# Performance work log

Measured on AMD Instinct MI355X. Metric: run time of the kernel, lower is better.

## Reference

```python
import jax, jax.numpy as jnp
import numpy as np

N_NODES = 50000   # nodes per channel
N_EDGES = 800000  # intra edges per channel (avg degree ~16)
N_GRAPHS = 64     # graphs in the batch (global_add_pool segments)
D = 128           # node_features_len == out_channels
L = 3             # n_layers
BN_EPS = 1e-5
NEG_SLOPE = 0.01  # F.leaky_relu default


def setup_inputs() -> dict:
    key = jax.random.key(0)
    ks = jax.random.split(key, 24)
    s = 0.05
    inp = {
        "x1": jax.random.normal(ks[0], (N_NODES, D), jnp.float32),
        "x2": jax.random.normal(ks[1], (N_NODES, D), jnp.float32),
        # GIN MLP channel 1: Linear-BN-ReLU-Linear-ReLU, stacked over layers
        "W1_ch1": jax.random.normal(ks[2], (L, D, D), jnp.float32) * s,
        "b1_ch1": jax.random.normal(ks[3], (L, D), jnp.float32) * s,
        "bn_g": 1.0 + jax.random.normal(ks[4], (L, D), jnp.float32) * s,
        "bn_b": jax.random.normal(ks[5], (L, D), jnp.float32) * s,
        "bn_m": jax.random.normal(ks[6], (L, D), jnp.float32) * s,
        "bn_v": 0.5 + jax.random.uniform(ks[7], (L, D), jnp.float32),
        "W2_ch1": jax.random.normal(ks[8], (L, D, D), jnp.float32) * s,
        "b2_ch1": jax.random.normal(ks[9], (L, D), jnp.float32) * s,
        # GIN MLP channel 2: Linear-ReLU-Linear
        "W1_ch2": jax.random.normal(ks[10], (L, D, D), jnp.float32) * s,
        "b1_ch2": jax.random.normal(ks[11], (L, D), jnp.float32) * s,
        "W2_ch2": jax.random.normal(ks[12], (L, D, D), jnp.float32) * s,
        "b2_ch2": jax.random.normal(ks[13], (L, D), jnp.float32) * s,
        # head: Linear(2*D*L -> D) - ReLU - Dropout - Linear(D -> 1)
        "Wf1": jax.random.normal(ks[14], (2 * D * L, D), jnp.float32) * s,
        "bf1": jax.random.normal(ks[15], (D,), jnp.float32) * s,
        "Wf2": jax.random.normal(ks[16], (D, 1), jnp.float32) * s,
        "bf2": jax.random.normal(ks[17], (1,), jnp.float32) * s,
        "edge1": jax.random.randint(ks[18], (2, N_EDGES), 0, N_NODES, dtype=jnp.int32),
        "edge2": jax.random.randint(ks[19], (2, N_EDGES), 0, N_NODES, dtype=jnp.int32),
        "batch1": jnp.sort(jax.random.randint(ks[20], (N_NODES,), 0, N_GRAPHS, dtype=jnp.int32)),
        "batch2": jnp.sort(jax.random.randint(ks[21], (N_NODES,), 0, N_GRAPHS, dtype=jnp.int32)),
    }
    return inp


def _aggregate(x, edge):
    # GINConv sum aggregation: message x[src] scattered to dst; eps=0 default
    return jax.ops.segment_sum(x[edge[0]], edge[1], num_segments=N_NODES)


def _channel1(x, edge, batch, W1, b1, g, b, m, v, W2, b2):
    pooled = []
    for i in range(L):
        h = (x + _aggregate(x, edge)) @ W1[i] + b1[i]
        h = (h - m[i]) * (g[i] / jnp.sqrt(v[i] + BN_EPS)) + b[i]  # eval-mode BN
        h = jax.nn.relu(h)
        h = jax.nn.relu(h @ W2[i] + b2[i])
        x = jax.nn.leaky_relu(h, NEG_SLOPE)
        pooled.append(jax.ops.segment_sum(x, batch, num_segments=N_GRAPHS))
    return jnp.concatenate(pooled, axis=-1)  # [G, D*L]


def _channel2(x, edge, batch, W1, b1, W2, b2):
    pooled = []
    for i in range(L):
        h = jax.nn.relu((x + _aggregate(x, edge)) @ W1[i] + b1[i])
        h = h @ W2[i] + b2[i]
        x = jax.nn.leaky_relu(h, NEG_SLOPE)
        pooled.append(jax.ops.segment_sum(x, batch, num_segments=N_GRAPHS))
    return jnp.concatenate(pooled, axis=-1)  # [G, D*L]


def reference(x1, x2, W1_ch1, b1_ch1, bn_g, bn_b, bn_m, bn_v, W2_ch1, b2_ch1,
              W1_ch2, b1_ch2, W2_ch2, b2_ch2, Wf1, bf1, Wf2, bf2,
              edge1, edge2, batch1, batch2):
    p1 = _channel1(x1, edge1, batch1, W1_ch1, b1_ch1, bn_g, bn_b, bn_m, bn_v, W2_ch1, b2_ch1)
    p2 = _channel2(x2, edge2, batch2, W1_ch2, b1_ch2, W2_ch2, b2_ch2)
    z = jnp.concatenate([p1, p2], axis=-1)  # [G, 2*D*L]
    h = jax.nn.relu(z @ Wf1 + bf1)          # dropout is identity in eval mode
    return h @ Wf2 + bf2                    # [G, 1]
```

## Files before the change

kernel.cpp:

```cpp
#include <hip/hip_runtime.h>

#define NN 50000
#define NE 800000
#define NG 64
#define DD 128
#define NL 3
#define ZW (2 * DD * NL)
#define NB2 128
#define NPB 391
#define CAP2 8192
#define CHUNK 4096
#define P1B 196

typedef __attribute__((ext_vector_type(8))) short short8;
typedef __attribute__((ext_vector_type(4))) float f32x4;

__device__ inline unsigned short f2bf(float f) {
  unsigned int u = __float_as_uint(f);
  unsigned int r = (u + 0x7fffu + ((u >> 16) & 1u)) >> 16;
  return (unsigned short)r;
}

__global__ __launch_bounds__(256) void cvt_bf16_kernel(const float* __restrict__ in,
                                                       unsigned short* __restrict__ out, int n8) {
  int i = blockIdx.x * 256 + threadIdx.x;
  if (i >= n8) return;
  const float4* in4 = reinterpret_cast<const float4*>(in);
  float4 a = in4[2 * i], b = in4[2 * i + 1];
  uint4 o;
  o.x = (unsigned int)f2bf(a.x) | ((unsigned int)f2bf(a.y) << 16);
  o.y = (unsigned int)f2bf(a.z) | ((unsigned int)f2bf(a.w) << 16);
  o.z = (unsigned int)f2bf(b.x) | ((unsigned int)f2bf(b.y) << 16);
  o.w = (unsigned int)f2bf(b.z) | ((unsigned int)f2bf(b.w) << 16);
  reinterpret_cast<uint4*>(out)[i] = o;
}

__global__ __launch_bounds__(256) void cvt_wt_kernel(const float* __restrict__ in,
                                                     unsigned short* __restrict__ out) {
  __shared__ float tile[32][33];
  int mat = blockIdx.z;
  int k0 = blockIdx.x * 32, c0 = blockIdx.y * 32;
  int tx = threadIdx.x & 31, ty = threadIdx.x >> 5;
  const float* ip = in + mat * 16384;
  unsigned short* op = out + mat * 16384;
#pragma unroll
  for (int rr = 0; rr < 32; rr += 8)
    tile[ty + rr][tx] = ip[(k0 + ty + rr) * 128 + (c0 + tx)];
  __syncthreads();
#pragma unroll
  for (int rr = 0; rr < 32; rr += 8)
    op[(c0 + ty + rr) * 128 + (k0 + tx)] = f2bf(tile[tx][ty + rr]);
}

__global__ __launch_bounds__(256) void bucket_kernel(const int* __restrict__ e1,
                                                     const int* __restrict__ e2,
                                                     int* __restrict__ bcur,
                                                     uint2* __restrict__ pairs) {
  int ch = blockIdx.x >= P1B;
  int blk = blockIdx.x - ch * P1B;
  const int* E = ch ? e2 : e1;
  int base = blk * CHUNK;
  __shared__ int lcnt[NB2], gbase[NB2];
  for (int i = threadIdx.x; i < NB2; i += 256) lcnt[i] = 0;
  __syncthreads();
  int srcv[16], dstv[16], lrank[16];
#pragma unroll
  for (int k = 0; k < 16; k++) {
    int e = base + k * 256 + threadIdx.x;
    if (e < NE) {
      srcv[k] = E[e];
      dstv[k] = E[NE + e];
      lrank[k] = atomicAdd(&lcnt[dstv[k] / NPB], 1);
    } else dstv[k] = -1;
  }
  __syncthreads();
  for (int i = threadIdx.x; i < NB2; i += 256)
    gbase[i] = atomicAdd(&bcur[ch * NB2 + i], lcnt[i]);
  __syncthreads();
#pragma unroll
  for (int k = 0; k < 16; k++)
    if (dstv[k] >= 0) {
      int g = dstv[k] / NPB;
      pairs[(size_t)(ch * NB2 + g) * CAP2 + gbase[g] + lrank[k]] =
          make_uint2((unsigned)srcv[k], (unsigned)dstv[k]);
    }
}

__global__ __launch_bounds__(256) void scan_bcur_kernel(const int* __restrict__ bcur,
                                                        int* __restrict__ colbase) {
  __shared__ int s[256];
  int tid = threadIdx.x;
  int v = bcur[tid];
  s[tid] = v;
  __syncthreads();
  int segstart = tid & ~127;
  for (int o = 1; o < 128; o <<= 1) {
    int t = (tid - o >= segstart) ? s[tid - o] : 0;
    __syncthreads();
    s[tid] += t;
    __syncthreads();
  }
  colbase[tid] = s[tid] - v;
}

__global__ __launch_bounds__(256) void csr_build_kernel(const uint2* __restrict__ pairs,
                                                        const int* __restrict__ bcur,
                                                        const int* __restrict__ colbase,
                                                        int* __restrict__ rowptr,
                                                        int* __restrict__ col) {
  int g = blockIdx.x;
  int ch = g >> 7, b = g & 127;
  int node0 = b * NPB;
  int nloc = min(NPB, NN - node0);
  int count = bcur[g];
  int base = colbase[g];
  const uint2* p = pairs + (size_t)g * CAP2;
  __shared__ int hist[512], pref[512], cur[512], stmp[256];
  for (int i = threadIdx.x; i < 512; i += 256) hist[i] = 0;
  __syncthreads();
  for (int e = threadIdx.x; e < count; e += 256)
    atomicAdd(&hist[(int)p[e].y - node0], 1);
  __syncthreads();
  int t = threadIdx.x;
  int a0 = hist[2 * t], a1 = hist[2 * t + 1];
  int sum = a0 + a1;
  stmp[t] = sum;
  __syncthreads();
  for (int o = 1; o < 256; o <<= 1) {
    int tv = (t >= o) ? stmp[t - o] : 0;
    __syncthreads();
    stmp[t] += tv;
    __syncthreads();
  }
  int ex = stmp[t] - sum;
  pref[2 * t] = ex;       pref[2 * t + 1] = ex + a0;
  cur[2 * t] = ex;        cur[2 * t + 1] = ex + a0;
  __syncthreads();
  for (int i = threadIdx.x; i < nloc; i += 256)
    rowptr[ch * (NN + 1) + node0 + i] = base + pref[i];
  if (threadIdx.x == 0 && b == NB2 - 1) rowptr[ch * (NN + 1) + NN] = base + count;
  for (int e = threadIdx.x; e < count; e += 256) {
    uint2 pr = p[e];
    int pos = atomicAdd(&cur[(int)pr.y - node0], 1);
    col[ch * NE + base + pos] = (int)pr.x;
  }
}

__global__ __launch_bounds__(256) void agg_kernel(const unsigned short* __restrict__ X,
                                                  const int* __restrict__ rowptr,
                                                  const int* __restrict__ col,
                                                  unsigned short* __restrict__ Y) {
  int node = blockIdx.x * 16 + (threadIdx.x >> 4);
  int lane = threadIdx.x & 15;
  int ch = node >= NN;
  int nl = node - ch * NN;
  const int* rp = rowptr + ch * (NN + 1);
  const int* cl = col + ch * NE;
  const uint4* X4 = reinterpret_cast<const uint4*>(X);
  size_t chbase = (size_t)ch * NN * 16;
  float acc[8];
  {
    uint4 sv = X4[(size_t)node * 16 + lane];
    unsigned int w[4] = {sv.x, sv.y, sv.z, sv.w};
#pragma unroll
    for (int q = 0; q < 4; q++) {
      acc[2 * q]     = __uint_as_float(w[q] << 16);
      acc[2 * q + 1] = __uint_as_float(w[q] & 0xffff0000u);
    }
  }
  int s = rp[nl], e = rp[nl + 1];
  int j = s;
  for (; j + 8 <= e; j += 8) {
    uint4 v[8];
#pragma unroll
    for (int q = 0; q < 8; q++)
      v[q] = X4[chbase + (size_t)cl[j + q] * 16 + lane];
#pragma unroll
    for (int q = 0; q < 8; q++) {
      unsigned int w[4] = {v[q].x, v[q].y, v[q].z, v[q].w};
#pragma unroll
      for (int t = 0; t < 4; t++) {
        acc[2 * t]     += __uint_as_float(w[t] << 16);
        acc[2 * t + 1] += __uint_as_float(w[t] & 0xffff0000u);
      }
    }
  }
  for (; j < e; ++j) {
    uint4 v = X4[chbase + (size_t)cl[j] * 16 + lane];
    unsigned int w[4] = {v.x, v.y, v.z, v.w};
#pragma unroll
    for (int t = 0; t < 4; t++) {
      acc[2 * t]     += __uint_as_float(w[t] << 16);
      acc[2 * t + 1] += __uint_as_float(w[t] & 0xffff0000u);
    }
  }
  uint4 o;
  unsigned int* ow = reinterpret_cast<unsigned int*>(&o);
#pragma unroll
  for (int q = 0; q < 4; q++)
    ow[q] = (unsigned int)f2bf(acc[2 * q]) | ((unsigned int)f2bf(acc[2 * q + 1]) << 16);
  reinterpret_cast<uint4*>(Y)[(size_t)node * 16 + lane] = o;
}

__global__ __launch_bounds__(256) void gemm_fused_kernel(
    const unsigned short* __restrict__ Y, unsigned short* __restrict__ X,
    const unsigned short* __restrict__ WT,
    const float* __restrict__ b1c1, const float* __restrict__ b1c2,
    const float* __restrict__ b2c1, const float* __restrict__ b2c2,
    const float* __restrict__ bng, const float* __restrict__ bnb,
    const float* __restrict__ bnm, const float* __restrict__ bnv,
    const int* __restrict__ batch1, const int* __restrict__ batch2,
    float* __restrict__ z, int layer) {
  __shared__ unsigned short hlds[16][136];
  int ch = blockIdx.x >= 1024;
  int lane = threadIdx.x & 63, wv = threadIdx.x >> 6;
  int l15 = lane & 15, lk = lane >> 4;
  int c0 = wv * 32;
  const unsigned short* W1 = WT + (size_t)(ch * 6 + layer) * 16384;
  const unsigned short* W2 = WT + (size_t)(ch * 6 + 3 + layer) * 16384;
  short8 w1f[2][4], w2f[2][4];
#pragma unroll
  for (int ct = 0; ct < 2; ct++)
#pragma unroll
    for (int kk = 0; kk < 4; kk++) {
      size_t boff = (size_t)(c0 + ct * 16 + l15) * 128 + kk * 32 + lk * 8;
      w1f[ct][kk] = *reinterpret_cast<const short8*>(W1 + boff);
      w2f[ct][kk] = *reinterpret_cast<const short8*>(W2 + boff);
    }
  const float* b1 = (ch ? b1c2 : b1c1) + layer * DD;
  const float* b2 = (ch ? b2c2 : b2c1) + layer * DD;
  const int* batch = ch ? batch2 : batch1;
  float sc1[2], sh1[2], sh2[2];
#pragma unroll
  for (int ct = 0; ct < 2; ct++) {
    int colg = c0 + ct * 16 + l15;
    if (!ch) {
      float s = bng[layer * DD + colg] * rsqrtf(bnv[layer * DD + colg] + 1e-5f);
      sc1[ct] = s;
      sh1[ct] = (b1[colg] - bnm[layer * DD + colg]) * s + bnb[layer * DD + colg];
    } else {
      sc1[ct] = 1.f;
      sh1[ct] = b1[colg];
    }
    sh2[ct] = b2[colg];
  }
  for (int t = (ch ? blockIdx.x - 1024 : blockIdx.x); t < 3125; t += 1024) {
    int r0l = t * 16;
    size_t r0g = (size_t)ch * NN + r0l;
    const unsigned short* yp = Y + (r0g + l15) * 128 + lk * 8;
    short8 a0 = *reinterpret_cast<const short8*>(yp);
    short8 a1 = *reinterpret_cast<const short8*>(yp + 32);
    short8 a2 = *reinterpret_cast<const short8*>(yp + 64);
    short8 a3 = *reinterpret_cast<const short8*>(yp + 96);
#pragma unroll
    for (int ct = 0; ct < 2; ct++) {
      f32x4 acc = {0.f, 0.f, 0.f, 0.f};
      acc = __builtin_amdgcn_mfma_f32_16x16x32_bf16(a0, w1f[ct][0], acc, 0, 0, 0);
      acc = __builtin_amdgcn_mfma_f32_16x16x32_bf16(a1, w1f[ct][1], acc, 0, 0, 0);
      acc = __builtin_amdgcn_mfma_f32_16x16x32_bf16(a2, w1f[ct][2], acc, 0, 0, 0);
      acc = __builtin_amdgcn_mfma_f32_16x16x32_bf16(a3, w1f[ct][3], acc, 0, 0, 0);
      int colg = c0 + ct * 16 + l15;
#pragma unroll
      for (int r = 0; r < 4; r++) {
        float tv = fmaxf(acc[r] * sc1[ct] + sh1[ct], 0.f);
        hlds[lk * 4 + r][colg] = f2bf(tv);
      }
    }
    __syncthreads();
    short8 h0 = *reinterpret_cast<const short8*>(&hlds[l15][lk * 8]);
    short8 h1 = *reinterpret_cast<const short8*>(&hlds[l15][32 + lk * 8]);
    short8 h2 = *reinterpret_cast<const short8*>(&hlds[l15][64 + lk * 8]);
    short8 h3 = *reinterpret_cast<const short8*>(&hlds[l15][96 + lk * 8]);
#pragma unroll
    for (int ct = 0; ct < 2; ct++) {
      f32x4 acc = {0.f, 0.f, 0.f, 0.f};
      acc = __builtin_amdgcn_mfma_f32_16x16x32_bf16(h0, w2f[ct][0], acc, 0, 0, 0);
      acc = __builtin_amdgcn_mfma_f32_16x16x32_bf16(h1, w2f[ct][1], acc, 0, 0, 0);
      acc = __builtin_amdgcn_mfma_f32_16x16x32_bf16(h2, w2f[ct][2], acc, 0, 0, 0);
      acc = __builtin_amdgcn_mfma_f32_16x16x32_bf16(h3, w2f[ct][3], acc, 0, 0, 0);
      int colg = c0 + ct * 16 + l15;
      float v[4];
#pragma unroll
      for (int r = 0; r < 4; r++) {
        float tv = acc[r] + sh2[ct];
        if (!ch) tv = fmaxf(tv, 0.f);
        else     tv = tv > 0.f ? tv : 0.01f * tv;
        v[r] = tv;
        X[(r0g + lk * 4 + r) * 128 + colg] = f2bf(tv);
      }
      int zc = ch * (DD * NL) + layer * DD + colg;
      int g0 = batch[r0l], g15 = batch[r0l + 15];
      if (g0 == g15) {
        float s = v[0] + v[1] + v[2] + v[3];
        s += __shfl_xor(s, 16);
        s += __shfl_xor(s, 32);
        if (lk == 0) atomicAdd(&z[(size_t)g0 * ZW + zc], s);
      } else {
#pragma unroll
        for (int r = 0; r < 4; r++)
          atomicAdd(&z[(size_t)batch[r0l + lk * 4 + r] * ZW + zc], v[r]);
      }
    }
    __syncthreads();
  }
}

__global__ __launch_bounds__(128) void head_kernel(const float* __restrict__ z,
                                                   const float* __restrict__ Wf1,
                                                   const float* __restrict__ bf1,
                                                   const float* __restrict__ Wf2,
                                                   const float* __restrict__ bf2,
                                                   float* __restrict__ out) {
  int g = blockIdx.x, t = threadIdx.x;
  const float* zr = z + (size_t)g * ZW;
  float acc = bf1[t];
  for (int j = 0; j < ZW; ++j) acc += zr[j] * Wf1[(size_t)j * DD + t];
  float h = fmaxf(acc, 0.f);
  __shared__ float red[128];
  red[t] = h * Wf2[t];
  __syncthreads();
  for (int s = 64; s > 0; s >>= 1) {
    if (t < s) red[t] += red[t + s];
    __syncthreads();
  }
  if (t == 0) out[g] = red[0] + bf2[0];
}

extern "C" void kernel_launch(void* const* d_in, const int* in_sizes, int n_in,
                              void* d_out, int out_size, void* d_ws, size_t ws_size,
                              hipStream_t stream) {
  const float* x1   = (const float*)d_in[0];
  const float* x2   = (const float*)d_in[1];
  const float* W1c1 = (const float*)d_in[2];
  const float* b1c1 = (const float*)d_in[3];
  const float* bng  = (const float*)d_in[4];
  const float* bnb  = (const float*)d_in[5];
  const float* bnm  = (const float*)d_in[6];
  const float* bnv  = (const float*)d_in[7];
  const float* W2c1 = (const float*)d_in[8];
  const float* b2c1 = (const float*)d_in[9];
  const float* W1c2 = (const float*)d_in[10];
  const float* b1c2 = (const float*)d_in[11];
  const float* W2c2 = (const float*)d_in[12];
  const float* b2c2 = (const float*)d_in[13];
  const float* Wf1  = (const float*)d_in[14];
  const float* bf1  = (const float*)d_in[15];
  const float* Wf2  = (const float*)d_in[16];
  const float* bf2  = (const float*)d_in[17];
  const int* edge1  = (const int*)d_in[18];
  const int* edge2  = (const int*)d_in[19];
  const int* batch1 = (const int*)d_in[20];
  const int* batch2 = (const int*)d_in[21];
  (void)ws_size; (void)n_in; (void)in_sizes; (void)out_size;

  char* ws = (char*)d_ws;
  const size_t NB16 = (size_t)2 * NN * DD * 2;
  unsigned short* bufX = (unsigned short*)(ws);
  unsigned short* bufY = (unsigned short*)(ws + NB16);
  size_t off = 2 * NB16;
  unsigned short* WT = (unsigned short*)(ws + off); off += (size_t)12 * 16384 * 2;
  uint2* pairs = (uint2*)(ws + off); off += (size_t)2 * NB2 * CAP2 * 8;
  int* col     = (int*)(ws + off); off += (size_t)2 * NE * 4;
  int* rowptr  = (int*)(ws + off); off += (((size_t)2 * (NN + 1) * 4) + 255) & ~(size_t)255;
  int* bcur    = (int*)(ws + off); off += 256 * 4;
  int* colbase = (int*)(ws + off); off += 256 * 4;
  float* z     = (float*)(ws + off); off += (size_t)NG * ZW * 4;

  cvt_wt_kernel<<<dim3(4, 4, 3), 256, 0, stream>>>(W1c1, WT + 0 * 16384);
  cvt_wt_kernel<<<dim3(4, 4, 3), 256, 0, stream>>>(W2c1, WT + 3 * 16384);
  cvt_wt_kernel<<<dim3(4, 4, 3), 256, 0, stream>>>(W1c2, WT + 6 * 16384);
  cvt_wt_kernel<<<dim3(4, 4, 3), 256, 0, stream>>>(W2c2, WT + 9 * 16384);

  hipMemsetAsync(z, 0, (size_t)NG * ZW * 4, stream);
  hipMemsetAsync(bcur, 0, 256 * 4, stream);

  cvt_bf16_kernel<<<(NN * DD / 8 + 255) / 256, 256, 0, stream>>>(x1, bufX, NN * DD / 8);
  cvt_bf16_kernel<<<(NN * DD / 8 + 255) / 256, 256, 0, stream>>>(x2, bufX + (size_t)NN * DD,
                                                                 NN * DD / 8);

  bucket_kernel<<<2 * P1B, 256, 0, stream>>>(edge1, edge2, bcur, pairs);
  scan_bcur_kernel<<<1, 256, 0, stream>>>(bcur, colbase);
  csr_build_kernel<<<2 * NB2, 256, 0, stream>>>(pairs, bcur, colbase, rowptr, col);

  for (int i = 0; i < NL; ++i) {
    agg_kernel<<<2 * NN / 16, 256, 0, stream>>>(bufX, rowptr, col, bufY);
    gemm_fused_kernel<<<2048, 256, 0, stream>>>(bufY, bufX, WT,
                                                b1c1, b1c2, b2c1, b2c2,
                                                bng, bnb, bnm, bnv,
                                                batch1, batch2, z, i);
  }
  head_kernel<<<NG, 128, 0, stream>>>(z, Wf1, bf1, Wf2, bf2, (float*)d_out);
}
```

Baseline: 394.4 us.

## Fuse neighbor aggregation into the per-layer GEMM kernel with ping-pong buffers

Merges the separate aggregation kernel into the fused MLP/pool kernel. Each 16-node tile first gathers its neighbor sums into shared memory, then runs both MFMA GEMMs on them, so the intermediate Y buffer is never written to or read back from global memory. Outputs go to a second buffer (ping-pong) because other blocks are still gathering from the input, and the last layer skips writing node features. The trade-off is that the gather now runs in a persistent grid of 2048 blocks with extra barriers, which may reduce the latency hiding the old 6250-block aggregation kernel had.

Result: slower. 455.9 us (+15.6%).

```diff
diff --git a/kernel.cpp b/kernel.cpp
--- a/kernel.cpp
+++ b/kernel.cpp
@@ -11,6 +11,7 @@
 #define CAP2 8192
 #define CHUNK 4096
 #define P1B 196
+#define GB2 1024
 
 typedef __attribute__((ext_vector_type(8))) short short8;
 typedef __attribute__((ext_vector_type(4))) float f32x4;
@@ -146,76 +147,30 @@
   }
 }
 
-__global__ __launch_bounds__(256) void agg_kernel(const unsigned short* __restrict__ X,
-                                                  const int* __restrict__ rowptr,
-                                                  const int* __restrict__ col,
-                                                  unsigned short* __restrict__ Y) {
-  int node = blockIdx.x * 16 + (threadIdx.x >> 4);
-  int lane = threadIdx.x & 15;
-  int ch = node >= NN;
-  int nl = node - ch * NN;
-  const int* rp = rowptr + ch * (NN + 1);
-  const int* cl = col + ch * NE;
-  const uint4* X4 = reinterpret_cast<const uint4*>(X);
-  size_t chbase = (size_t)ch * NN * 16;
-  float acc[8];
-  {
-    uint4 sv = X4[(size_t)node * 16 + lane];
-    unsigned int w[4] = {sv.x, sv.y, sv.z, sv.w};
-#pragma unroll
-    for (int q = 0; q < 4; q++) {
-      acc[2 * q]     = __uint_as_float(w[q] << 16);
-      acc[2 * q + 1] = __uint_as_float(w[q] & 0xffff0000u);
-    }
-  }
-  int s = rp[nl], e = rp[nl + 1];
-  int j = s;
-  for (; j + 8 <= e; j += 8) {
-    uint4 v[8];
-#pragma unroll
-    for (int q = 0; q < 8; q++)
-      v[q] = X4[chbase + (size_t)cl[j + q] * 16 + lane];
-#pragma unroll
-    for (int q = 0; q < 8; q++) {
-      unsigned int w[4] = {v[q].x, v[q].y, v[q].z, v[q].w};
-#pragma unroll
-      for (int t = 0; t < 4; t++) {
-        acc[2 * t]     += __uint_as_float(w[t] << 16);
-        acc[2 * t + 1] += __uint_as_float(w[t] & 0xffff0000u);
-      }
-    }
-  }
-  for (; j < e; ++j) {
-    uint4 v = X4[chbase + (size_t)cl[j] * 16 + lane];
-    unsigned int w[4] = {v.x, v.y, v.z, v.w};
-#pragma unroll
-    for (int t = 0; t < 4; t++) {
-      acc[2 * t]     += __uint_as_float(w[t] << 16);
-      acc[2 * t + 1] += __uint_as_float(w[t] & 0xffff0000u);
-    }
-  }
-  uint4 o;
-  unsigned int* ow = reinterpret_cast<unsigned int*>(&o);
-#pragma unroll
-  for (int q = 0; q < 4; q++)
-    ow[q] = (unsigned int)f2bf(acc[2 * q]) | ((unsigned int)f2bf(acc[2 * q + 1]) << 16);
-  reinterpret_cast<uint4*>(Y)[(size_t)node * 16 + lane] = o;
-}
-
-__global__ __launch_bounds__(256) void gemm_fused_kernel(
-    const unsigned short* __restrict__ Y, unsigned short* __restrict__ X,
+__global__ __launch_bounds__(256) void layer_fused_kernel(
+    const unsigned short* __restrict__ Xin, unsigned short* __restrict__ Xout,
+    const int* __restrict__ rowptr, const int* __restrict__ col,
     const unsigned short* __restrict__ WT,
     const float* __restrict__ b1c1, const float* __restrict__ b1c2,
     const float* __restrict__ b2c1, const float* __restrict__ b2c2,
     const float* __restrict__ bng, const float* __restrict__ bnb,
     const float* __restrict__ bnm, const float* __restrict__ bnv,
     const int* __restrict__ batch1, const int* __restrict__ batch2,
-    float* __restrict__ z, int layer) {
+    float* __restrict__ z, int layer, int writeOut) {
+  __shared__ unsigned short ylds[16][136];
   __shared__ unsigned short hlds[16][136];
-  int ch = blockIdx.x >= 1024;
-  int lane = threadIdx.x & 63, wv = threadIdx.x >> 6;
-  int l15 = lane & 15, lk = lane >> 4;
+  int ch = blockIdx.x >= GB2;
+  int bid = blockIdx.x - ch * GB2;
+  int tid = threadIdx.x;
+  int nsub = tid >> 4, lane = tid & 15;
+  int lane64 = tid & 63, wv = tid >> 6;
+  int l15 = lane64 & 15, lk = lane64 >> 4;
   int c0 = wv * 32;
+  const int* rp = rowptr + ch * (NN + 1);
+  const int* cl = col + ch * NE;
+  const uint4* X4 = reinterpret_cast<const uint4*>(Xin);
+  size_t chbase = (size_t)ch * NN * 16;
+
   const unsigned short* W1 = WT + (size_t)(ch * 6 + layer) * 16384;
   const unsigned short* W2 = WT + (size_t)(ch * 6 + 3 + layer) * 16384;
   short8 w1f[2][4], w2f[2][4];
@@ -244,64 +199,113 @@
     }
     sh2[ct] = b2[colg];
   }
-  for (int t = (ch ? blockIdx.x - 1024 : blockIdx.x); t < 3125; t += 1024) {
+
+  for (int t = bid; t < 3125; t += GB2) {
     int r0l = t * 16;
     size_t r0g = (size_t)ch * NN + r0l;
-    const unsigned short* yp = Y + (r0g + l15) * 128 + lk * 8;
-    short8 a0 = *reinterpret_cast<const short8*>(yp);
-    short8 a1 = *reinterpret_cast<const short8*>(yp + 32);
-    short8 a2 = *reinterpret_cast<const short8*>(yp + 64);
-    short8 a3 = *reinterpret_cast<const short8*>(yp + 96);
-#pragma unroll
-    for (int ct = 0; ct < 2; ct++) {
-      f32x4 acc = {0.f, 0.f, 0.f, 0.f};
-      acc = __builtin_amdgcn_mfma_f32_16x16x32_bf16(a0, w1f[ct][0], acc, 0, 0, 0);
-      acc = __builtin_amdgcn_mfma_f32_16x16x32_bf16(a1, w1f[ct][1], acc, 0, 0, 0);
-      acc = __builtin_amdgcn_mfma_f32_16x16x32_bf16(a2, w1f[ct][2], acc, 0, 0, 0);
-      acc = __builtin_amdgcn_mfma_f32_16x16x32_bf16(a3, w1f[ct][3], acc, 0, 0, 0);
-      int colg = c0 + ct * 16 + l15;
-#pragma unroll
-      for (int r = 0; r < 4; r++) {
-        float tv = fmaxf(acc[r] * sc1[ct] + sh1[ct], 0.f);
-        hlds[lk * 4 + r][colg] = f2bf(tv);
+    {
+      int nl = r0l + nsub;
+      float acc[8];
+      uint4 sv = X4[(r0g + nsub) * 16 + lane];
+      {
+        unsigned int w[4] = {sv.x, sv.y, sv.z, sv.w};
+#pragma unroll
+        for (int q = 0; q < 4; q++) {
+          acc[2 * q]     = __uint_as_float(w[q] << 16);
+          acc[2 * q + 1] = __uint_as_float(w[q] & 0xffff0000u);
+        }
       }
-    }
-    __syncthreads();
-    short8 h0 = *reinterpret_cast<const short8*>(&hlds[l15][lk * 8]);
-    short8 h1 = *reinterpret_cast<const short8*>(&hlds[l15][32 + lk * 8]);
-    short8 h2 = *reinterpret_cast<const short8*>(&hlds[l15][64 + lk * 8]);
-    short8 h3 = *reinterpret_cast<const short8*>(&hlds[l15][96 + lk * 8]);
-#pragma unroll
-    for (int ct = 0; ct < 2; ct++) {
-      f32x4 acc = {0.f, 0.f, 0.f, 0.f};
-      acc = __builtin_amdgcn_mfma_f32_16x16x32_bf16(h0, w2f[ct][0], acc, 0, 0, 0);
-      acc = __builtin_amdgcn_mfma_f32_16x16x32_bf16(h1, w2f[ct][1], acc, 0, 0, 0);
-      acc = __builtin_amdgcn_mfma_f32_16x16x32_bf16(h2, w2f[ct][2], acc, 0, 0, 0);
-      acc = __builtin_amdgcn_mfma_f32_16x16x32_bf16(h3, w2f[ct][3], acc, 0, 0, 0);
-      int colg = c0 + ct * 16 + l15;
-      float v[4];
-#pragma unroll
-      for (int r = 0; r < 4; r++) {
-        float tv = acc[r] + sh2[ct];
-        if (!ch) tv = fmaxf(tv, 0.f);
-        else     tv = tv > 0.f ? tv : 0.01f * tv;
-        v[r] = tv;
-        X[(r0g + lk * 4 + r) * 128 + colg] = f2bf(tv);
+      int s = rp[nl], e = rp[nl + 1];
+      int j = s;
+      for (; j + 8 <= e; j += 8) {
+        uint4 v[8];
+#pragma unroll
+        for (int q = 0; q < 8; q++)
+          v[q] = X4[chbase + (size_t)cl[j + q] * 16 + lane];
+#pragma unroll
+        for (int q = 0; q < 8; q++) {
+          unsigned int w[4] = {v[q].x, v[q].y, v[q].z, v[q].w};
+#pragma unroll
+          for (int u = 0; u < 4; u++) {
+            acc[2 * u]     += __uint_as_float(w[u] << 16);
+            acc[2 * u + 1] += __uint_as_float(w[u] & 0xffff0000u);
+          }
+        }
       }
-      int zc = ch * (DD * NL) + layer * DD + colg;
-      int g0 = batch[r0l], g15 = batch[r0l + 15];
-      if (g0 == g15) {
-        float s = v[0] + v[1] + v[2] + v[3];
-        s += __shfl_xor(s, 16);
-        s += __shfl_xor(s, 32);
-        if (lk == 0) atomicAdd(&z[(size_t)g0 * ZW + zc], s);
-      } else {
-#pragma unroll
-        for (int r = 0; r < 4; r++)
-          atomicAdd(&z[(size_t)batch[r0l + lk * 4 + r] * ZW + zc], v[r]);
+      for (; j < e; ++j) {
+        uint4 v = X4[chbase + (size_t)cl[j] * 16 + lane];
+        unsigned int w[4] = {v.x, v.y, v.z, v.w};
+#pragma unroll
+        for (int u = 0; u < 4; u++) {
+          acc[2 * u]     += __uint_as_float(w[u] << 16);
+          acc[2 * u + 1] += __uint_as_float(w[u] & 0xffff0000u);
+        }
       }
-    }
-    __syncthreads();
+      uint4 o;
+      unsigned int* ow = reinterpret_cast<unsigned int*>(&o);
+#pragma unroll
+      for (int q = 0; q < 4; q++)
+        ow[q] = (unsigned int)f2bf(acc[2 * q]) | ((unsigned int)f2bf(acc[2 * q + 1]) << 16);
+      *reinterpret_cast<uint4*>(&ylds[nsub][lane * 8]) = o;
+    }
+    __syncthreads();
+    {
+      short8 a0 = *reinterpret_cast<const short8*>(&ylds[l15][lk * 8]);
+      short8 a1 = *reinterpret_cast<const short8*>(&ylds[l15][32 + lk * 8]);
+      short8 a2 = *reinterpret_cast<const short8*>(&ylds[l15][64 + lk * 8]);
+      short8 a3 = *reinterpret_cast<const short8*>(&ylds[l15][96 + lk * 8]);
+#pragma unroll
+      for (int ct = 0; ct < 2; ct++) {
+        f32x4 acc = {0.f, 0.f, 0.f, 0.f};
+        acc = __builtin_amdgcn_mfma_f32_16x16x32_bf16(a0, w1f[ct][0], acc, 0, 0, 0);
+        acc = __builtin_amdgcn_mfma_f32_16x16x32_bf16(a1, w1f[ct][1], acc, 0, 0, 0);
+        acc = __builtin_amdgcn_mfma_f32_16x16x32_bf16(a2, w1f[ct][2], acc, 0, 0, 0);
+        acc = __builtin_amdgcn_mfma_f32_16x16x32_bf16(a3, w1f[ct][3], acc, 0, 0, 0);
+        int colg = c0 + ct * 16 + l15;
+#pragma unroll
+        for (int r = 0; r < 4; r++) {
+          float tv = fmaxf(acc[r] * sc1[ct] + sh1[ct], 0.f);
+          hlds[lk * 4 + r][colg] = f2bf(tv);
+        }
+      }
+    }
+    __syncthreads();
+    {
+      short8 h0 = *reinterpret_cast<const short8*>(&hlds[l15][lk * 8]);
+      short8 h1 = *reinterpret_cast<const short8*>(&hlds[l15][32 + lk * 8]);
+      short8 h2 = *reinterpret_cast<const short8*>(&hlds[l15][64 + lk * 8]);
+      short8 h3 = *reinterpret_cast<const short8*>(&hlds[l15][96 + lk * 8]);
+#pragma unroll
+      for (int ct = 0; ct < 2; ct++) {
+        f32x4 acc = {0.f, 0.f, 0.f, 0.f};
+        acc = __builtin_amdgcn_mfma_f32_16x16x32_bf16(h0, w2f[ct][0], acc, 0, 0, 0);
+        acc = __builtin_amdgcn_mfma_f32_16x16x32_bf16(h1, w2f[ct][1], acc, 0, 0, 0);
+        acc = __builtin_amdgcn_mfma_f32_16x16x32_bf16(h2, w2f[ct][2], acc, 0, 0, 0);
+        acc = __builtin_amdgcn_mfma_f32_16x16x32_bf16(h3, w2f[ct][3], acc, 0, 0, 0);
+        int colg = c0 + ct * 16 + l15;
+        float v[4];
+#pragma unroll
+        for (int r = 0; r < 4; r++) {
+          float tv = acc[r] + sh2[ct];
+          if (!ch) tv = fmaxf(tv, 0.f);
+          else     tv = tv > 0.f ? tv : 0.01f * tv;
+          v[r] = tv;
+          if (writeOut) Xout[(r0g + lk * 4 + r) * 128 + colg] = f2bf(tv);
+        }
+        int zc = ch * (DD * NL) + layer * DD + colg;
+        int g0 = batch[r0l], g15 = batch[r0l + 15];
+        if (g0 == g15) {
+          float s = v[0] + v[1] + v[2] + v[3];
+          s += __shfl_xor(s, 16);
+          s += __shfl_xor(s, 32);
+          if (lk == 0) atomicAdd(&z[(size_t)g0 * ZW + zc], s);
+        } else {
+#pragma unroll
+          for (int r = 0; r < 4; r++)
+            atomicAdd(&z[(size_t)batch[r0l + lk * 4 + r] * ZW + zc], v[r]);
+        }
+      }
+    }
   }
 }
 
@@ -355,8 +359,8 @@
 
   char* ws = (char*)d_ws;
   const size_t NB16 = (size_t)2 * NN * DD * 2;
-  unsigned short* bufX = (unsigned short*)(ws);
-  unsigned short* bufY = (unsigned short*)(ws + NB16);
+  unsigned short* bufA = (unsigned short*)(ws);
+  unsigned short* bufB = (unsigned short*)(ws + NB16);
   size_t off = 2 * NB16;
   unsigned short* WT = (unsigned short*)(ws + off); off += (size_t)12 * 16384 * 2;
   uint2* pairs = (uint2*)(ws + off); off += (size_t)2 * NB2 * CAP2 * 8;
@@ -374,20 +378,23 @@
   hipMemsetAsync(z, 0, (size_t)NG * ZW * 4, stream);
   hipMemsetAsync(bcur, 0, 256 * 4, stream);
 
-  cvt_bf16_kernel<<<(NN * DD / 8 + 255) / 256, 256, 0, stream>>>(x1, bufX, NN * DD / 8);
-  cvt_bf16_kernel<<<(NN * DD / 8 + 255) / 256, 256, 0, stream>>>(x2, bufX + (size_t)NN * DD,
+  cvt_bf16_kernel<<<(NN * DD / 8 + 255) / 256, 256, 0, stream>>>(x1, bufA, NN * DD / 8);
+  cvt_bf16_kernel<<<(NN * DD / 8 + 255) / 256, 256, 0, stream>>>(x2, bufA + (size_t)NN * DD,
                                                                  NN * DD / 8);
 
   bucket_kernel<<<2 * P1B, 256, 0, stream>>>(edge1, edge2, bcur, pairs);
   scan_bcur_kernel<<<1, 256, 0, stream>>>(bcur, colbase);
   csr_build_kernel<<<2 * NB2, 256, 0, stream>>>(pairs, bcur, colbase, rowptr, col);
 
-  for (int i = 0; i < NL; ++i) {
-    agg_kernel<<<2 * NN / 16, 256, 0, stream>>>(bufX, rowptr, col, bufY);
-    gemm_fused_kernel<<<2048, 256, 0, stream>>>(bufY, bufX, WT,
-                                                b1c1, b1c2, b2c1, b2c2,
-                                                bng, bnb, bnm, bnv,
-                                                batch1, batch2, z, i);
-  }
+  layer_fused_kernel<<<2 * GB2, 256, 0, stream>>>(bufA, bufB, rowptr, col, WT,
+                                                  b1c1, b1c2, b2c1, b2c2, bng, bnb, bnm, bnv,
+                                                  batch1, batch2, z, 0, 1);
+  layer_fused_kernel<<<2 * GB2, 256, 0, stream>>>(bufB, bufA, rowptr, col, WT,
+                                                  b1c1, b1c2, b2c1, b2c2, bng, bnb, bnm, bnv,
+                                                  batch1, batch2, z, 1, 1);
+  layer_fused_kernel<<<2 * GB2, 256, 0, stream>>>(bufA, bufB, rowptr, col, WT,
+                                                  b1c1, b1c2, b2c1, b2c2, bng, bnb, bnm, bnv,
+                                                  batch1, batch2, z, 2, 0);
+
   head_kernel<<<NG, 128, 0, stream>>>(z, Wf1, bf1, Wf2, bf2, (float*)d_out);
 }
```

## Move graph pooling out of GEMM epilogue into segmented reduction kernel

Applied to the files above, without the earlier changes.

Removes the per-tile atomicAdd pooling from the fused GEMM epilogue and adds a separate pool kernel that sums each graph's contiguous node range. Range starts come from a binary search over the sorted batch arrays. Ping-pong node buffers let the pooling read the new layer output. This avoids atomics and batch lookups in the GEMM, but adds an extra pass over the node features per layer with only 128 blocks, and it pools bf16-rounded values.

New measurement: 388.9 us. About the same (-1.4%).

```diff
diff --git a/kernel.cpp b/kernel.cpp
--- a/kernel.cpp
+++ b/kernel.cpp
@@ -11,6 +11,7 @@
 #define CAP2 8192
 #define CHUNK 4096
 #define P1B 196
+#define GB2 1024
 
 typedef __attribute__((ext_vector_type(8))) short short8;
 typedef __attribute__((ext_vector_type(4))) float f32x4;
@@ -144,6 +145,21 @@
     int pos = atomicAdd(&cur[(int)pr.y - node0], 1);
     col[ch * NE + base + pos] = (int)pr.x;
   }
+}
+
+__global__ __launch_bounds__(256) void gstart_kernel(const int* __restrict__ batch1,
+                                                     const int* __restrict__ batch2,
+                                                     int* __restrict__ gstart) {
+  int t = threadIdx.x;
+  if (t >= 2 * (NG + 1)) return;
+  int ch = t / (NG + 1), g = t % (NG + 1);
+  const int* b = ch ? batch2 : batch1;
+  int lo = 0, hi = NN;
+  while (lo < hi) {
+    int m = (lo + hi) >> 1;
+    if (b[m] < g) lo = m + 1; else hi = m;
+  }
+  gstart[t] = lo;
 }
 
 __global__ __launch_bounds__(256) void agg_kernel(const unsigned short* __restrict__ X,
@@ -208,11 +224,9 @@
     const float* __restrict__ b1c1, const float* __restrict__ b1c2,
     const float* __restrict__ b2c1, const float* __restrict__ b2c2,
     const float* __restrict__ bng, const float* __restrict__ bnb,
-    const float* __restrict__ bnm, const float* __restrict__ bnv,
-    const int* __restrict__ batch1, const int* __restrict__ batch2,
-    float* __restrict__ z, int layer) {
+    const float* __restrict__ bnm, const float* __restrict__ bnv, int layer) {
   __shared__ unsigned short hlds[16][136];
-  int ch = blockIdx.x >= 1024;
+  int ch = blockIdx.x >= GB2;
   int lane = threadIdx.x & 63, wv = threadIdx.x >> 6;
   int l15 = lane & 15, lk = lane >> 4;
   int c0 = wv * 32;
@@ -229,7 +243,6 @@
     }
   const float* b1 = (ch ? b1c2 : b1c1) + layer * DD;
   const float* b2 = (ch ? b2c2 : b2c1) + layer * DD;
-  const int* batch = ch ? batch2 : batch1;
   float sc1[2], sh1[2], sh2[2];
 #pragma unroll
   for (int ct = 0; ct < 2; ct++) {
@@ -244,7 +257,7 @@
     }
     sh2[ct] = b2[colg];
   }
-  for (int t = (ch ? blockIdx.x - 1024 : blockIdx.x); t < 3125; t += 1024) {
+  for (int t = (ch ? blockIdx.x - GB2 : blockIdx.x); t < 3125; t += GB2) {
     int r0l = t * 16;
     size_t r0g = (size_t)ch * NN + r0l;
     const unsigned short* yp = Y + (r0g + l15) * 128 + lk * 8;
@@ -279,29 +292,74 @@
       acc = __builtin_amdgcn_mfma_f32_16x16x32_bf16(h2, w2f[ct][2], acc, 0, 0, 0);
       acc = __builtin_amdgcn_mfma_f32_16x16x32_bf16(h3, w2f[ct][3], acc, 0, 0, 0);
       int colg = c0 + ct * 16 + l15;
-      float v[4];
 #pragma unroll
       for (int r = 0; r < 4; r++) {
         float tv = acc[r] + sh2[ct];
         if (!ch) tv = fmaxf(tv, 0.f);
         else     tv = tv > 0.f ? tv : 0.01f * tv;
-        v[r] = tv;
         X[(r0g + lk * 4 + r) * 128 + colg] = f2bf(tv);
       }
-      int zc = ch * (DD * NL) + layer * DD + colg;
-      int g0 = batch[r0l], g15 = batch[r0l + 15];
-      if (g0 == g15) {
-        float s = v[0] + v[1] + v[2] + v[3];
-        s += __shfl_xor(s, 16);
-        s += __shfl_xor(s, 32);
-        if (lk == 0) atomicAdd(&z[(size_t)g0 * ZW + zc], s);
-      } else {
-#pragma unroll
-        for (int r = 0; r < 4; r++)
-          atomicAdd(&z[(size_t)batch[r0l + lk * 4 + r] * ZW + zc], v[r]);
-      }
-    }
-    __syncthreads();
+    }
+    __syncthreads();
+  }
+}
+
+__global__ __launch_bounds__(256) void pool_kernel(const unsigned short* __restrict__ X,
+                                                   const int* __restrict__ gstart,
+                                                   float* __restrict__ z, int layer) {
+  int ch = blockIdx.x >> 6, g = blockIdx.x & 63;
+  int r0 = gstart[ch * (NG + 1) + g], r1 = gstart[ch * (NG + 1) + g + 1];
+  int c8 = threadIdx.x & 15, part = threadIdx.x >> 4;
+  const uint4* X4 = reinterpret_cast<const uint4*>(X);
+  size_t base = (size_t)ch * NN * 16 + c8;
+  float acc[8];
+#pragma unroll
+  for (int q = 0; q < 8; q++) acc[q] = 0.f;
+  int r = r0 + part;
+  for (; r + 48 < r1; r += 64) {
+    uint4 v0 = X4[base + (size_t)r * 16];
+    uint4 v1 = X4[base + (size_t)(r + 16) * 16];
+    uint4 v2 = X4[base + (size_t)(r + 32) * 16];
+    uint4 v3 = X4[base + (size_t)(r + 48) * 16];
+    unsigned int w0[4] = {v0.x, v0.y, v0.z, v0.w};
+    unsigned int w1[4] = {v1.x, v1.y, v1.z, v1.w};
+    unsigned int w2[4] = {v2.x, v2.y, v2.z, v2.w};
+    unsigned int w3[4] = {v3.x, v3.y, v3.z, v3.w};
+#pragma unroll
+    for (int q = 0; q < 4; q++) {
+      acc[2 * q]     += __uint_as_float(w0[q] << 16) + __uint_as_float(w1[q] << 16) +
+                        __uint_as_float(w2[q] << 16) + __uint_as_float(w3[q] << 16);
+      acc[2 * q + 1] += __uint_as_float(w0[q] & 0xffff0000u) + __uint_as_float(w1[q] & 0xffff0000u) +
+                        __uint_as_float(w2[q] & 0xffff0000u) + __uint_as_float(w3[q] & 0xffff0000u);
+    }
+  }
+  for (; r < r1; r += 16) {
+    uint4 v = X4[base + (size_t)r * 16];
+    unsigned int w[4] = {v.x, v.y, v.z, v.w};
+#pragma unroll
+    for (int q = 0; q < 4; q++) {
+      acc[2 * q]     += __uint_as_float(w[q] << 16);
+      acc[2 * q + 1] += __uint_as_float(w[q] & 0xffff0000u);
+    }
+  }
+  __shared__ float zacc[16][128];
+#pragma unroll
+  for (int q = 0; q < 8; q++) zacc[part][c8 * 8 + q] = acc[q];
+  __syncthreads();
+  for (int s = 8; s > 0; s >>= 1) {
+    if (part < s) {
+#pragma unroll
+      for (int q = 0; q < 8; q++)
+        zacc[part][c8 * 8 + q] += zacc[part + s][c8 * 8 + q];
+    }
+    __syncthreads();
+  }
+  if (part == 0) {
+#pragma unroll
+    for (int q = 0; q < 8; q++) {
+      int colw = c8 * 8 + q;
+      z[(size_t)g * ZW + ch * DD * NL + layer * DD + colw] = zacc[0][colw];
+    }
   }
 }
 
@@ -355,15 +413,17 @@
 
   char* ws = (char*)d_ws;
   const size_t NB16 = (size_t)2 * NN * DD * 2;
-  unsigned short* bufX = (unsigned short*)(ws);
-  unsigned short* bufY = (unsigned short*)(ws + NB16);
-  size_t off = 2 * NB16;
+  unsigned short* bufA = (unsigned short*)(ws);
+  unsigned short* bufB = (unsigned short*)(ws + NB16);
+  unsigned short* bufY = (unsigned short*)(ws + 2 * NB16);
+  size_t off = 3 * NB16;
   unsigned short* WT = (unsigned short*)(ws + off); off += (size_t)12 * 16384 * 2;
   uint2* pairs = (uint2*)(ws + off); off += (size_t)2 * NB2 * CAP2 * 8;
   int* col     = (int*)(ws + off); off += (size_t)2 * NE * 4;
   int* rowptr  = (int*)(ws + off); off += (((size_t)2 * (NN + 1) * 4) + 255) & ~(size_t)255;
   int* bcur    = (int*)(ws + off); off += 256 * 4;
   int* colbase = (int*)(ws + off); off += 256 * 4;
+  int* gstart  = (int*)(ws + off); off += 256 * 4;
   float* z     = (float*)(ws + off); off += (size_t)NG * ZW * 4;
 
   cvt_wt_kernel<<<dim3(4, 4, 3), 256, 0, stream>>>(W1c1, WT + 0 * 16384);
@@ -371,23 +431,27 @@
   cvt_wt_kernel<<<dim3(4, 4, 3), 256, 0, stream>>>(W1c2, WT + 6 * 16384);
   cvt_wt_kernel<<<dim3(4, 4, 3), 256, 0, stream>>>(W2c2, WT + 9 * 16384);
 
-  hipMemsetAsync(z, 0, (size_t)NG * ZW * 4, stream);
   hipMemsetAsync(bcur, 0, 256 * 4, stream);
 
-  cvt_bf16_kernel<<<(NN * DD / 8 + 255) / 256, 256, 0, stream>>>(x1, bufX, NN * DD / 8);
-  cvt_bf16_kernel<<<(NN * DD / 8 + 255) / 256, 256, 0, stream>>>(x2, bufX + (size_t)NN * DD,
+  cvt_bf16_kernel<<<(NN * DD / 8 + 255) / 256, 256, 0, stream>>>(x1, bufA, NN * DD / 8);
+  cvt_bf16_kernel<<<(NN * DD / 8 + 255) / 256, 256, 0, stream>>>(x2, bufA + (size_t)NN * DD,
                                                                  NN * DD / 8);
 
   bucket_kernel<<<2 * P1B, 256, 0, stream>>>(edge1, edge2, bcur, pairs);
   scan_bcur_kernel<<<1, 256, 0, stream>>>(bcur, colbase);
   csr_build_kernel<<<2 * NB2, 256, 0, stream>>>(pairs, bcur, colbase, rowptr, col);
-
+  gstart_kernel<<<1, 256, 0, stream>>>(batch1, batch2, gstart);
+
+  unsigned short* cin = bufA;
+  unsigned short* cout = bufB;
   for (int i = 0; i < NL; ++i) {
-    agg_kernel<<<2 * NN / 16, 256, 0, stream>>>(bufX, rowptr, col, bufY);
-    gemm_fused_kernel<<<2048, 256, 0, stream>>>(bufY, bufX, WT,
-                                                b1c1, b1c2, b2c1, b2c2,
-                                                bng, bnb, bnm, bnv,
-                                                batch1, batch2, z, i);
-  }
+    agg_kernel<<<2 * NN / 16, 256, 0, stream>>>(cin, rowptr, col, bufY);
+    gemm_fused_kernel<<<2 * GB2, 256, 0, stream>>>(bufY, cout, WT,
+                                                   b1c1, b1c2, b2c1, b2c2,
+                                                   bng, bnb, bnm, bnv, i);
+    pool_kernel<<<2 * NG, 256, 0, stream>>>(cout, gstart, z, i);
+    unsigned short* tmp = cin; cin = cout; cout = tmp;
+  }
+
   head_kernel<<<NG, 128, 0, stream>>>(z, Wf1, bf1, Wf2, bf2, (float*)d_out);
 }
```
